# Kernel optimization log

Hardware: AMD Instinct MI355X
Metric: run time of the kernel (lower is better)

## Reference

```python
import jax, jax.numpy as jnp
import numpy as np

N_NODES = 100000
N_EDGES = 600000
D_FEAT = 128
OUT_DIM = 128


def setup_inputs() -> dict:
    key = jax.random.key(0)
    k_x, k_r, k_c, k_v, k_w = jax.random.split(key, 5)
    x = jax.random.normal(k_x, (N_NODES, D_FEAT), dtype=jnp.float32)
    adj_rows = jax.random.randint(k_r, (N_EDGES,), 0, N_NODES, dtype=jnp.int64 if jax.config.jax_enable_x64 else jnp.int32).astype(jnp.int32)
    adj_cols = jax.random.randint(k_c, (N_EDGES,), 0, N_NODES, dtype=jnp.int32)
    adj_vals = jax.random.uniform(k_v, (N_EDGES,), dtype=jnp.float32)
    # Xavier-uniform init for W of shape [2*d, out]
    fan_in, fan_out = 2 * D_FEAT, OUT_DIM
    bound = float(np.sqrt(6.0 / (fan_in + fan_out)))
    W = jax.random.uniform(k_w, (2 * D_FEAT, OUT_DIM), minval=-bound, maxval=bound, dtype=jnp.float32)
    return {"x": x, "adj_rows": adj_rows, "adj_cols": adj_cols, "adj_vals": adj_vals, "W": W}


def reference(x, adj_rows, adj_cols, adj_vals, W):
    # h = A @ x  via COO SpMM: gather neighbor features, scale, segment-sum by row
    msgs = adj_vals[:, None] * x[adj_cols]            # [E, d]
    h = jax.ops.segment_sum(msgs, adj_rows, num_segments=N_NODES)  # [N, d]
    # concat([h, x]) @ W == h @ W[:d] + x @ W[d:]  (avoids materializing concat)
    out = h @ W[:D_FEAT] + x @ W[D_FEAT:]             # [N, out]
    return jax.nn.relu(out)
```

## Files before the change

kernel.cpp:

```cpp
#include <hip/hip_runtime.h>
#include <hip/hip_bf16.h>

constexpr int N_NODES = 100000;
constexpr int N_EDGES = 600000;
constexpr int D = 128;
constexpr int CAP = 32;

constexpr size_t X16_OFF  = 0;
constexpr size_t WP_OFF   = 25600000;
constexpr size_t CNT_OFF  = 25665536;
constexpr size_t BINS_OFF = 26065536;

typedef __attribute__((ext_vector_type(8))) short short8;
typedef __attribute__((ext_vector_type(4))) float float4v;
typedef __attribute__((ext_vector_type(4))) float float4e;
typedef __attribute__((ext_vector_type(4))) int   int4e;

__device__ inline unsigned short f2bf(float f) {
    union { float f; unsigned int u; } v; v.f = f;
    unsigned int u = v.u + 0x7fffu + ((v.u >> 16) & 1u);
    return (unsigned short)(u >> 16);
}
__device__ inline float bf2f(unsigned int lo16) {
    union { unsigned int u; float f; } v; v.u = lo16 << 16;
    return v.f;
}

__global__ __launch_bounds__(256) void prep_cast_kernel(
    const float* __restrict__ x, uint4* __restrict__ x16,
    const float* __restrict__ W, unsigned short* __restrict__ Wp)
{
    const int tid = blockIdx.x * 256 + threadIdx.x;
    const int T   = gridDim.x * 256;

    for (int idx = tid; idx < 8 * 8 * 64 * 8; idx += T) {
        int j    = idx & 7;
        int lane = (idx >> 3) & 63;
        int jt   = (idx >> 9) & 7;
        int s    = idx >> 12;
        int k = s * 32 + (lane >> 4) * 8 + j;
        int n = jt * 16 + (lane & 15);
        Wp[idx] = f2bf(W[k * 128 + n]);
    }

    for (int g = tid; g < N_NODES * D / 8; g += T) {
        const float4e* xp = reinterpret_cast<const float4e*>(x + (size_t)g * 8);
        float4e a = __builtin_nontemporal_load(xp);
        float4e c = __builtin_nontemporal_load(xp + 1);
        uint4 o;
        o.x = (unsigned int)f2bf(a.x) | ((unsigned int)f2bf(a.y) << 16);
        o.y = (unsigned int)f2bf(a.z) | ((unsigned int)f2bf(a.w) << 16);
        o.z = (unsigned int)f2bf(c.x) | ((unsigned int)f2bf(c.y) << 16);
        o.w = (unsigned int)f2bf(c.z) | ((unsigned int)f2bf(c.w) << 16);
        x16[g] = o;
    }
}

__global__ __launch_bounds__(256) void prep_bin_kernel(
    const int* __restrict__ rows, const int* __restrict__ cols,
    const float* __restrict__ vals,
    int* __restrict__ cnt, int2* __restrict__ bins)
{
    const int tid = blockIdx.x * 256 + threadIdx.x;
    const int T   = gridDim.x * 256;

    for (int e = tid; e < N_EDGES; e += T) {
        int r = __builtin_nontemporal_load(rows + e);
        int c = __builtin_nontemporal_load(cols + e);
        float v = __builtin_nontemporal_load(vals + e);
        int pos = atomicAdd(&cnt[r], 1);
        if (pos < CAP)
            bins[(size_t)r * CAP + pos] = make_int2(c, __float_as_int(v));
    }
}

__global__ __launch_bounds__(256) void fused_agg_gemm_kernel(
    const uint4* __restrict__ x16v,
    const unsigned short* __restrict__ x16s,
    const int* __restrict__ cnt,
    const int2* __restrict__ bins,
    const unsigned short* __restrict__ Wp,
    float* __restrict__ out)
{
    __shared__ uint4 lds4[256];

    const int tid  = threadIdx.x;
    const int wave = tid >> 6;
    const int lane = tid & 63;
    const int row0 = blockIdx.x * 16;

    {
        const int G  = wave * 4 + (lane >> 4);
        const int gl = lane & 15;
        const int n  = row0 + G;

        const int4e* b2 = reinterpret_cast<const int4e*>(bins + (size_t)n * CAP);
        const int  d   = cnt[n];
        const int4e c0 = __builtin_nontemporal_load(b2 + 0);
        const int4e c1 = __builtin_nontemporal_load(b2 + 1);
        const int4e c2 = __builtin_nontemporal_load(b2 + 2);
        const int4e c3 = __builtin_nontemporal_load(b2 + 3);
        const int dend = d > CAP ? CAP : d;

        int col0 = c0.x; col0 = col0 < 0 ? 0 : col0;
        col0 = col0 >= N_NODES ? N_NODES - 1 : col0;
        const int cc1 = (1 < dend) ? c0.z : col0;
        const int cc2 = (2 < dend) ? c1.x : col0;
        const int cc3 = (3 < dend) ? c1.z : col0;
        const int cc4 = (4 < dend) ? c2.x : col0;
        const int cc5 = (5 < dend) ? c2.z : col0;
        const int cc6 = (6 < dend) ? c3.x : col0;
        const int cc7 = (7 < dend) ? c3.z : col0;
        const float v0 = (0 < dend) ? __int_as_float(c0.y) : 0.f;
        const float v1 = (1 < dend) ? __int_as_float(c0.w) : 0.f;
        const float v2 = (2 < dend) ? __int_as_float(c1.y) : 0.f;
        const float v3 = (3 < dend) ? __int_as_float(c1.w) : 0.f;
        const float v4 = (4 < dend) ? __int_as_float(c2.y) : 0.f;
        const float v5 = (5 < dend) ? __int_as_float(c2.w) : 0.f;
        const float v6 = (6 < dend) ? __int_as_float(c3.y) : 0.f;
        const float v7 = (7 < dend) ? __int_as_float(c3.w) : 0.f;

        const uint4 p0 = x16v[(size_t)col0 * 16 + gl];
        const uint4 p1 = x16v[(size_t)cc1  * 16 + gl];
        const uint4 p2 = x16v[(size_t)cc2  * 16 + gl];
        const uint4 p3 = x16v[(size_t)cc3  * 16 + gl];
        const uint4 p4 = x16v[(size_t)cc4  * 16 + gl];
        const uint4 p5 = x16v[(size_t)cc5  * 16 + gl];
        const uint4 p6 = x16v[(size_t)cc6  * 16 + gl];
        const uint4 p7 = x16v[(size_t)cc7  * 16 + gl];

        float a0, a1, a2, a3, a4, a5, a6, a7;
        a0  = v0 * bf2f(p0.x & 0xffffu) + v1 * bf2f(p1.x & 0xffffu)
            + v2 * bf2f(p2.x & 0xffffu) + v3 * bf2f(p3.x & 0xffffu)
            + v4 * bf2f(p4.x & 0xffffu) + v5 * bf2f(p5.x & 0xffffu)
            + v6 * bf2f(p6.x & 0xffffu) + v7 * bf2f(p7.x & 0xffffu);
        a1  = v0 * bf2f(p0.x >> 16)     + v1 * bf2f(p1.x >> 16)
            + v2 * bf2f(p2.x >> 16)     + v3 * bf2f(p3.x >> 16)
            + v4 * bf2f(p4.x >> 16)     + v5 * bf2f(p5.x >> 16)
            + v6 * bf2f(p6.x >> 16)     + v7 * bf2f(p7.x >> 16);
        a2  = v0 * bf2f(p0.y & 0xffffu) + v1 * bf2f(p1.y & 0xffffu)
            + v2 * bf2f(p2.y & 0xffffu) + v3 * bf2f(p3.y & 0xffffu)
            + v4 * bf2f(p4.y & 0xffffu) + v5 * bf2f(p5.y & 0xffffu)
            + v6 * bf2f(p6.y & 0xffffu) + v7 * bf2f(p7.y & 0xffffu);
        a3  = v0 * bf2f(p0.y >> 16)     + v1 * bf2f(p1.y >> 16)
            + v2 * bf2f(p2.y >> 16)     + v3 * bf2f(p3.y >> 16)
            + v4 * bf2f(p4.y >> 16)     + v5 * bf2f(p5.y >> 16)
            + v6 * bf2f(p6.y >> 16)     + v7 * bf2f(p7.y >> 16);
        a4  = v0 * bf2f(p0.z & 0xffffu) + v1 * bf2f(p1.z & 0xffffu)
            + v2 * bf2f(p2.z & 0xffffu) + v3 * bf2f(p3.z & 0xffffu)
            + v4 * bf2f(p4.z & 0xffffu) + v5 * bf2f(p5.z & 0xffffu)
            + v6 * bf2f(p6.z & 0xffffu) + v7 * bf2f(p7.z & 0xffffu);
        a5  = v0 * bf2f(p0.z >> 16)     + v1 * bf2f(p1.z >> 16)
            + v2 * bf2f(p2.z >> 16)     + v3 * bf2f(p3.z >> 16)
            + v4 * bf2f(p4.z >> 16)     + v5 * bf2f(p5.z >> 16)
            + v6 * bf2f(p6.z >> 16)     + v7 * bf2f(p7.z >> 16);
        a6  = v0 * bf2f(p0.w & 0xffffu) + v1 * bf2f(p1.w & 0xffffu)
            + v2 * bf2f(p2.w & 0xffffu) + v3 * bf2f(p3.w & 0xffffu)
            + v4 * bf2f(p4.w & 0xffffu) + v5 * bf2f(p5.w & 0xffffu)
            + v6 * bf2f(p6.w & 0xffffu) + v7 * bf2f(p7.w & 0xffffu);
        a7  = v0 * bf2f(p0.w >> 16)     + v1 * bf2f(p1.w >> 16)
            + v2 * bf2f(p2.w >> 16)     + v3 * bf2f(p3.w >> 16)
            + v4 * bf2f(p4.w >> 16)     + v5 * bf2f(p5.w >> 16)
            + v6 * bf2f(p6.w >> 16)     + v7 * bf2f(p7.w >> 16);

        if (dend > 8) {
            const int2* bp = bins + (size_t)n * CAP;
            for (int i = 8; i < dend; i += 4) {
                const int i1 = (i + 1 < dend) ? i + 1 : dend - 1;
                const int i2 = (i + 2 < dend) ? i + 2 : dend - 1;
                const int i3 = (i + 3 < dend) ? i + 3 : dend - 1;
                int2 e0 = bp[i];
                int2 e1 = bp[i1];
                int2 e2 = bp[i2];
                int2 e3 = bp[i3];
                uint4 q0 = x16v[(size_t)e0.x * 16 + gl];
                uint4 q1 = x16v[(size_t)e1.x * 16 + gl];
                uint4 q2 = x16v[(size_t)e2.x * 16 + gl];
                uint4 q3 = x16v[(size_t)e3.x * 16 + gl];
                float w0 = __int_as_float(e0.y);
                float w1 = (i + 1 < dend) ? __int_as_float(e1.y) : 0.f;
                float w2 = (i + 2 < dend) ? __int_as_float(e2.y) : 0.f;
                float w3 = (i + 3 < dend) ? __int_as_float(e3.y) : 0.f;
                a0 += w0 * bf2f(q0.x & 0xffffu) + w1 * bf2f(q1.x & 0xffffu)
                    + w2 * bf2f(q2.x & 0xffffu) + w3 * bf2f(q3.x & 0xffffu);
                a1 += w0 * bf2f(q0.x >> 16)     + w1 * bf2f(q1.x >> 16)
                    + w2 * bf2f(q2.x >> 16)     + w3 * bf2f(q3.x >> 16);
                a2 += w0 * bf2f(q0.y & 0xffffu) + w1 * bf2f(q1.y & 0xffffu)
                    + w2 * bf2f(q2.y & 0xffffu) + w3 * bf2f(q3.y & 0xffffu);
                a3 += w0 * bf2f(q0.y >> 16)     + w1 * bf2f(q1.y >> 16)
                    + w2 * bf2f(q2.y >> 16)     + w3 * bf2f(q3.y >> 16);
                a4 += w0 * bf2f(q0.z & 0xffffu) + w1 * bf2f(q1.z & 0xffffu)
                    + w2 * bf2f(q2.z & 0xffffu) + w3 * bf2f(q3.z & 0xffffu);
                a5 += w0 * bf2f(q0.z >> 16)     + w1 * bf2f(q1.z >> 16)
                    + w2 * bf2f(q2.z >> 16)     + w3 * bf2f(q3.z >> 16);
                a6 += w0 * bf2f(q0.w & 0xffffu) + w1 * bf2f(q1.w & 0xffffu)
                    + w2 * bf2f(q2.w & 0xffffu) + w3 * bf2f(q3.w & 0xffffu);
                a7 += w0 * bf2f(q0.w >> 16)     + w1 * bf2f(q1.w >> 16)
                    + w2 * bf2f(q2.w >> 16)     + w3 * bf2f(q3.w >> 16);
            }
        }

        uint4 o;
        o.x = (unsigned int)f2bf(a0) | ((unsigned int)f2bf(a1) << 16);
        o.y = (unsigned int)f2bf(a2) | ((unsigned int)f2bf(a3) << 16);
        o.z = (unsigned int)f2bf(a4) | ((unsigned int)f2bf(a5) << 16);
        o.w = (unsigned int)f2bf(a6) | ((unsigned int)f2bf(a7) << 16);
        lds4[(gl >> 2) * 64 + G * 4 + (gl & 3)] = o;
    }
    __syncthreads();

    const int m    = lane & 15;
    const int quad = lane >> 4;
    const int jt0  = wave * 2;
    const int jt1  = jt0 + 1;

    const unsigned short* xrow = x16s + (size_t)(row0 + m) * D + quad * 8;

    float4v acc0 = (float4v){0.f, 0.f, 0.f, 0.f};
    float4v acc1 = (float4v){0.f, 0.f, 0.f, 0.f};

    #pragma unroll
    for (int s = 0; s < 8; s++) {
        short8 a;
        if (s < 4)
            a = *reinterpret_cast<const short8*>(&lds4[s * 64 + m * 4 + quad]);
        else
            a = *reinterpret_cast<const short8*>(xrow + (s - 4) * 32);
        short8 b0 = *reinterpret_cast<const short8*>(
            Wp + ((size_t)((s * 8 + jt0) * 64 + lane)) * 8);
        short8 b1 = *reinterpret_cast<const short8*>(
            Wp + ((size_t)((s * 8 + jt1) * 64 + lane)) * 8);
        acc0 = __builtin_amdgcn_mfma_f32_16x16x32_bf16(a, b0, acc0, 0, 0, 0);
        acc1 = __builtin_amdgcn_mfma_f32_16x16x32_bf16(a, b1, acc1, 0, 0, 0);
    }

    #pragma unroll
    for (int reg = 0; reg < 4; reg++) {
        const int r = row0 + quad * 4 + reg;
        float* orow = out + (size_t)r * D;
        __builtin_nontemporal_store(fmaxf(acc0[reg], 0.f), orow + jt0 * 16 + m);
        __builtin_nontemporal_store(fmaxf(acc1[reg], 0.f), orow + jt1 * 16 + m);
    }
}

extern "C" void kernel_launch(void* const* d_in, const int* in_sizes, int n_in,
                              void* d_out, int out_size, void* d_ws, size_t ws_size,
                              hipStream_t stream)
{
    const float* x    = (const float*)d_in[0];
    const int*   rows = (const int*)  d_in[1];
    const int*   cols = (const int*)  d_in[2];
    const float* vals = (const float*)d_in[3];
    const float* W    = (const float*)d_in[4];
    float* out = (float*)d_out;

    char* ws = (char*)d_ws;
    uint4*          x16v = (uint4*)         (ws + X16_OFF);
    unsigned short* x16s = (unsigned short*)(ws + X16_OFF);
    unsigned short* Wp   = (unsigned short*)(ws + WP_OFF);
    int*            cnt  = (int*)           (ws + CNT_OFF);
    int2*           bins = (int2*)          (ws + BINS_OFF);

    hipMemsetAsync(cnt, 0, N_NODES * sizeof(int), stream);
    prep_cast_kernel<<<2048, 256, 0, stream>>>(x, x16v, W, Wp);
    prep_bin_kernel<<<2048, 256, 0, stream>>>(rows, cols, vals, cnt, bins);
    fused_agg_gemm_kernel<<<N_NODES / 16, 256, 0, stream>>>(
        x16v, x16s, cnt, bins, Wp, out);
}
```

Measured before the change: 197.3 us.

## Merge binning and aggregation into a persistent kernel with a grid barrier

The separate memset, binning and fused aggregate+GEMM launches become two kernels. The count zeroing moves into the prep kernel, and binning plus aggregation/GEMM run in one persistent kernel of 1024 blocks, joined by a software grid-wide barrier built on atomics. This is meant to remove launch overhead and kernel boundaries. In exchange, correctness depends on all 1024 blocks being co-resident (launch bounds of 4 blocks per CU are requested), the spin-wait barrier adds cost, and the tile loop now uses fewer blocks than the previous 6250-block launch.

```diff
diff --git a/kernel.cpp b/kernel.cpp
--- a/kernel.cpp
+++ b/kernel.cpp
@@ -5,11 +5,13 @@
 constexpr int N_EDGES = 600000;
 constexpr int D = 128;
 constexpr int CAP = 32;
+constexpr int NB2 = 1024;
 
 constexpr size_t X16_OFF  = 0;
 constexpr size_t WP_OFF   = 25600000;
 constexpr size_t CNT_OFF  = 25665536;
 constexpr size_t BINS_OFF = 26065536;
+constexpr size_t BAR_OFF  = 51665536;
 
 typedef __attribute__((ext_vector_type(8))) short short8;
 typedef __attribute__((ext_vector_type(4))) float float4v;
@@ -26,12 +28,16 @@
     return v.f;
 }
 
-__global__ __launch_bounds__(256) void prep_cast_kernel(
+__global__ __launch_bounds__(256) void prep_kernel(
     const float* __restrict__ x, uint4* __restrict__ x16,
-    const float* __restrict__ W, unsigned short* __restrict__ Wp)
+    const float* __restrict__ W, unsigned short* __restrict__ Wp,
+    int* __restrict__ cnt, int* __restrict__ bar)
 {
     const int tid = blockIdx.x * 256 + threadIdx.x;
     const int T   = gridDim.x * 256;
+
+    if (tid < 2) bar[tid] = 0;
+    for (int i = tid; i < N_NODES; i += T) cnt[i] = 0;
 
     for (int idx = tid; idx < 8 * 8 * 64 * 8; idx += T) {
         int j    = idx & 7;
@@ -56,13 +62,18 @@
     }
 }
 
-__global__ __launch_bounds__(256) void prep_bin_kernel(
+__global__ __launch_bounds__(256, 4) void work_kernel(
     const int* __restrict__ rows, const int* __restrict__ cols,
     const float* __restrict__ vals,
-    int* __restrict__ cnt, int2* __restrict__ bins)
+    const uint4* __restrict__ x16v, const unsigned short* __restrict__ x16s,
+    const unsigned short* __restrict__ Wp,
+    int* __restrict__ cnt, int2* __restrict__ bins,
+    int* __restrict__ bar, float* __restrict__ out)
 {
+    __shared__ uint4 lds4[256];
+
     const int tid = blockIdx.x * 256 + threadIdx.x;
-    const int T   = gridDim.x * 256;
+    const int T   = NB2 * 256;
 
     for (int e = tid; e < N_EDGES; e += T) {
         int r = __builtin_nontemporal_load(rows + e);
@@ -72,174 +83,184 @@
         if (pos < CAP)
             bins[(size_t)r * CAP + pos] = make_int2(c, __float_as_int(v));
     }
-}
-
-__global__ __launch_bounds__(256) void fused_agg_gemm_kernel(
-    const uint4* __restrict__ x16v,
-    const unsigned short* __restrict__ x16s,
-    const int* __restrict__ cnt,
-    const int2* __restrict__ bins,
-    const unsigned short* __restrict__ Wp,
-    float* __restrict__ out)
-{
-    __shared__ uint4 lds4[256];
-
-    const int tid  = threadIdx.x;
-    const int wave = tid >> 6;
-    const int lane = tid & 63;
-    const int row0 = blockIdx.x * 16;
-
-    {
-        const int G  = wave * 4 + (lane >> 4);
-        const int gl = lane & 15;
-        const int n  = row0 + G;
-
-        const int4e* b2 = reinterpret_cast<const int4e*>(bins + (size_t)n * CAP);
-        const int  d   = cnt[n];
-        const int4e c0 = __builtin_nontemporal_load(b2 + 0);
-        const int4e c1 = __builtin_nontemporal_load(b2 + 1);
-        const int4e c2 = __builtin_nontemporal_load(b2 + 2);
-        const int4e c3 = __builtin_nontemporal_load(b2 + 3);
-        const int dend = d > CAP ? CAP : d;
-
-        int col0 = c0.x; col0 = col0 < 0 ? 0 : col0;
-        col0 = col0 >= N_NODES ? N_NODES - 1 : col0;
-        const int cc1 = (1 < dend) ? c0.z : col0;
-        const int cc2 = (2 < dend) ? c1.x : col0;
-        const int cc3 = (3 < dend) ? c1.z : col0;
-        const int cc4 = (4 < dend) ? c2.x : col0;
-        const int cc5 = (5 < dend) ? c2.z : col0;
-        const int cc6 = (6 < dend) ? c3.x : col0;
-        const int cc7 = (7 < dend) ? c3.z : col0;
-        const float v0 = (0 < dend) ? __int_as_float(c0.y) : 0.f;
-        const float v1 = (1 < dend) ? __int_as_float(c0.w) : 0.f;
-        const float v2 = (2 < dend) ? __int_as_float(c1.y) : 0.f;
-        const float v3 = (3 < dend) ? __int_as_float(c1.w) : 0.f;
-        const float v4 = (4 < dend) ? __int_as_float(c2.y) : 0.f;
-        const float v5 = (5 < dend) ? __int_as_float(c2.w) : 0.f;
-        const float v6 = (6 < dend) ? __int_as_float(c3.y) : 0.f;
-        const float v7 = (7 < dend) ? __int_as_float(c3.w) : 0.f;
-
-        const uint4 p0 = x16v[(size_t)col0 * 16 + gl];
-        const uint4 p1 = x16v[(size_t)cc1  * 16 + gl];
-        const uint4 p2 = x16v[(size_t)cc2  * 16 + gl];
-        const uint4 p3 = x16v[(size_t)cc3  * 16 + gl];
-        const uint4 p4 = x16v[(size_t)cc4  * 16 + gl];
-        const uint4 p5 = x16v[(size_t)cc5  * 16 + gl];
-        const uint4 p6 = x16v[(size_t)cc6  * 16 + gl];
-        const uint4 p7 = x16v[(size_t)cc7  * 16 + gl];
-
-        float a0, a1, a2, a3, a4, a5, a6, a7;
-        a0  = v0 * bf2f(p0.x & 0xffffu) + v1 * bf2f(p1.x & 0xffffu)
-            + v2 * bf2f(p2.x & 0xffffu) + v3 * bf2f(p3.x & 0xffffu)
-            + v4 * bf2f(p4.x & 0xffffu) + v5 * bf2f(p5.x & 0xffffu)
-            + v6 * bf2f(p6.x & 0xffffu) + v7 * bf2f(p7.x & 0xffffu);
-        a1  = v0 * bf2f(p0.x >> 16)     + v1 * bf2f(p1.x >> 16)
-            + v2 * bf2f(p2.x >> 16)     + v3 * bf2f(p3.x >> 16)
-            + v4 * bf2f(p4.x >> 16)     + v5 * bf2f(p5.x >> 16)
-            + v6 * bf2f(p6.x >> 16)     + v7 * bf2f(p7.x >> 16);
-        a2  = v0 * bf2f(p0.y & 0xffffu) + v1 * bf2f(p1.y & 0xffffu)
-            + v2 * bf2f(p2.y & 0xffffu) + v3 * bf2f(p3.y & 0xffffu)
-            + v4 * bf2f(p4.y & 0xffffu) + v5 * bf2f(p5.y & 0xffffu)
-            + v6 * bf2f(p6.y & 0xffffu) + v7 * bf2f(p7.y & 0xffffu);
-        a3  = v0 * bf2f(p0.y >> 16)     + v1 * bf2f(p1.y >> 16)
-            + v2 * bf2f(p2.y >> 16)     + v3 * bf2f(p3.y >> 16)
-            + v4 * bf2f(p4.y >> 16)     + v5 * bf2f(p5.y >> 16)
-            + v6 * bf2f(p6.y >> 16)     + v7 * bf2f(p7.y >> 16);
-        a4  = v0 * bf2f(p0.z & 0xffffu) + v1 * bf2f(p1.z & 0xffffu)
-            + v2 * bf2f(p2.z & 0xffffu) + v3 * bf2f(p3.z & 0xffffu)
-            + v4 * bf2f(p4.z & 0xffffu) + v5 * bf2f(p5.z & 0xffffu)
-            + v6 * bf2f(p6.z & 0xffffu) + v7 * bf2f(p7.z & 0xffffu);
-        a5  = v0 * bf2f(p0.z >> 16)     + v1 * bf2f(p1.z >> 16)
-            + v2 * bf2f(p2.z >> 16)     + v3 * bf2f(p3.z >> 16)
-            + v4 * bf2f(p4.z >> 16)     + v5 * bf2f(p5.z >> 16)
-            + v6 * bf2f(p6.z >> 16)     + v7 * bf2f(p7.z >> 16);
-        a6  = v0 * bf2f(p0.w & 0xffffu) + v1 * bf2f(p1.w & 0xffffu)
-            + v2 * bf2f(p2.w & 0xffffu) + v3 * bf2f(p3.w & 0xffffu)
-            + v4 * bf2f(p4.w & 0xffffu) + v5 * bf2f(p5.w & 0xffffu)
-            + v6 * bf2f(p6.w & 0xffffu) + v7 * bf2f(p7.w & 0xffffu);
-        a7  = v0 * bf2f(p0.w >> 16)     + v1 * bf2f(p1.w >> 16)
-            + v2 * bf2f(p2.w >> 16)     + v3 * bf2f(p3.w >> 16)
-            + v4 * bf2f(p4.w >> 16)     + v5 * bf2f(p5.w >> 16)
-            + v6 * bf2f(p6.w >> 16)     + v7 * bf2f(p7.w >> 16);
-
-        if (dend > 8) {
-            const int2* bp = bins + (size_t)n * CAP;
-            for (int i = 8; i < dend; i += 4) {
-                const int i1 = (i + 1 < dend) ? i + 1 : dend - 1;
-                const int i2 = (i + 2 < dend) ? i + 2 : dend - 1;
-                const int i3 = (i + 3 < dend) ? i + 3 : dend - 1;
-                int2 e0 = bp[i];
-                int2 e1 = bp[i1];
-                int2 e2 = bp[i2];
-                int2 e3 = bp[i3];
-                uint4 q0 = x16v[(size_t)e0.x * 16 + gl];
-                uint4 q1 = x16v[(size_t)e1.x * 16 + gl];
-                uint4 q2 = x16v[(size_t)e2.x * 16 + gl];
-                uint4 q3 = x16v[(size_t)e3.x * 16 + gl];
-                float w0 = __int_as_float(e0.y);
-                float w1 = (i + 1 < dend) ? __int_as_float(e1.y) : 0.f;
-                float w2 = (i + 2 < dend) ? __int_as_float(e2.y) : 0.f;
-                float w3 = (i + 3 < dend) ? __int_as_float(e3.y) : 0.f;
-                a0 += w0 * bf2f(q0.x & 0xffffu) + w1 * bf2f(q1.x & 0xffffu)
-                    + w2 * bf2f(q2.x & 0xffffu) + w3 * bf2f(q3.x & 0xffffu);
-                a1 += w0 * bf2f(q0.x >> 16)     + w1 * bf2f(q1.x >> 16)
-                    + w2 * bf2f(q2.x >> 16)     + w3 * bf2f(q3.x >> 16);
-                a2 += w0 * bf2f(q0.y & 0xffffu) + w1 * bf2f(q1.y & 0xffffu)
-                    + w2 * bf2f(q2.y & 0xffffu) + w3 * bf2f(q3.y & 0xffffu);
-                a3 += w0 * bf2f(q0.y >> 16)     + w1 * bf2f(q1.y >> 16)
-                    + w2 * bf2f(q2.y >> 16)     + w3 * bf2f(q3.y >> 16);
-                a4 += w0 * bf2f(q0.z & 0xffffu) + w1 * bf2f(q1.z & 0xffffu)
-                    + w2 * bf2f(q2.z & 0xffffu) + w3 * bf2f(q3.z & 0xffffu);
-                a5 += w0 * bf2f(q0.z >> 16)     + w1 * bf2f(q1.z >> 16)
-                    + w2 * bf2f(q2.z >> 16)     + w3 * bf2f(q3.z >> 16);
-                a6 += w0 * bf2f(q0.w & 0xffffu) + w1 * bf2f(q1.w & 0xffffu)
-                    + w2 * bf2f(q2.w & 0xffffu) + w3 * bf2f(q3.w & 0xffffu);
-                a7 += w0 * bf2f(q0.w >> 16)     + w1 * bf2f(q1.w >> 16)
-                    + w2 * bf2f(q2.w >> 16)     + w3 * bf2f(q3.w >> 16);
+
+    __syncthreads();
+    if (threadIdx.x == 0) {
+        __threadfence();
+        int t = atomicAdd(&bar[0], 1);
+        if (t == NB2 - 1) {
+            __hip_atomic_store(&bar[1], 1, __ATOMIC_RELEASE,
+                               __HIP_MEMORY_SCOPE_AGENT);
+        } else {
+            while (__hip_atomic_load(&bar[1], __ATOMIC_RELAXED,
+                                     __HIP_MEMORY_SCOPE_AGENT) == 0)
+                __builtin_amdgcn_s_sleep(10);
+        }
+    }
+    __syncthreads();
+    __threadfence();
+
+    const int wave = threadIdx.x >> 6;
+    const int lane = threadIdx.x & 63;
+
+    for (int tile = blockIdx.x; tile < N_NODES / 16; tile += NB2) {
+        const int row0 = tile * 16;
+
+        {
+            const int G  = wave * 4 + (lane >> 4);
+            const int gl = lane & 15;
+            const int n  = row0 + G;
+
+            const int4e* b2 = reinterpret_cast<const int4e*>(bins + (size_t)n * CAP);
+            const int  d   = cnt[n];
+            const int4e c0 = __builtin_nontemporal_load(b2 + 0);
+            const int4e c1 = __builtin_nontemporal_load(b2 + 1);
+            const int4e c2 = __builtin_nontemporal_load(b2 + 2);
+            const int4e c3 = __builtin_nontemporal_load(b2 + 3);
+            const int dend = d > CAP ? CAP : d;
+
+            int col0 = c0.x; col0 = col0 < 0 ? 0 : col0;
+            col0 = col0 >= N_NODES ? N_NODES - 1 : col0;
+            const int cc1 = (1 < dend) ? c0.z : col0;
+            const int cc2 = (2 < dend) ? c1.x : col0;
+            const int cc3 = (3 < dend) ? c1.z : col0;
+            const int cc4 = (4 < dend) ? c2.x : col0;
+            const int cc5 = (5 < dend) ? c2.z : col0;
+            const int cc6 = (6 < dend) ? c3.x : col0;
+            const int cc7 = (7 < dend) ? c3.z : col0;
+            const float v0 = (0 < dend) ? __int_as_float(c0.y) : 0.f;
+            const float v1 = (1 < dend) ? __int_as_float(c0.w) : 0.f;
+            const float v2 = (2 < dend) ? __int_as_float(c1.y) : 0.f;
+            const float v3 = (3 < dend) ? __int_as_float(c1.w) : 0.f;
+            const float v4 = (4 < dend) ? __int_as_float(c2.y) : 0.f;
+            const float v5 = (5 < dend) ? __int_as_float(c2.w) : 0.f;
+            const float v6 = (6 < dend) ? __int_as_float(c3.y) : 0.f;
+            const float v7 = (7 < dend) ? __int_as_float(c3.w) : 0.f;
+
+            const uint4 p0 = x16v[(size_t)col0 * 16 + gl];
+            const uint4 p1 = x16v[(size_t)cc1  * 16 + gl];
+            const uint4 p2 = x16v[(size_t)cc2  * 16 + gl];
+            const uint4 p3 = x16v[(size_t)cc3  * 16 + gl];
+            const uint4 p4 = x16v[(size_t)cc4  * 16 + gl];
+            const uint4 p5 = x16v[(size_t)cc5  * 16 + gl];
+            const uint4 p6 = x16v[(size_t)cc6  * 16 + gl];
+            const uint4 p7 = x16v[(size_t)cc7  * 16 + gl];
+
+            float a0, a1, a2, a3, a4, a5, a6, a7;
+            a0  = v0 * bf2f(p0.x & 0xffffu) + v1 * bf2f(p1.x & 0xffffu)
+                + v2 * bf2f(p2.x & 0xffffu) + v3 * bf2f(p3.x & 0xffffu)
+                + v4 * bf2f(p4.x & 0xffffu) + v5 * bf2f(p5.x & 0xffffu)
+                + v6 * bf2f(p6.x & 0xffffu) + v7 * bf2f(p7.x & 0xffffu);
+            a1  = v0 * bf2f(p0.x >> 16)     + v1 * bf2f(p1.x >> 16)
+                + v2 * bf2f(p2.x >> 16)     + v3 * bf2f(p3.x >> 16)
+                + v4 * bf2f(p4.x >> 16)     + v5 * bf2f(p5.x >> 16)
+                + v6 * bf2f(p6.x >> 16)     + v7 * bf2f(p7.x >> 16);
+            a2  = v0 * bf2f(p0.y & 0xffffu) + v1 * bf2f(p1.y & 0xffffu)
+                + v2 * bf2f(p2.y & 0xffffu) + v3 * bf2f(p3.y & 0xffffu)
+                + v4 * bf2f(p4.y & 0xffffu) + v5 * bf2f(p5.y & 0xffffu)
+                + v6 * bf2f(p6.y & 0xffffu) + v7 * bf2f(p7.y & 0xffffu);
+            a3  = v0 * bf2f(p0.y >> 16)     + v1 * bf2f(p1.y >> 16)
+                + v2 * bf2f(p2.y >> 16)     + v3 * bf2f(p3.y >> 16)
+                + v4 * bf2f(p4.y >> 16)     + v5 * bf2f(p5.y >> 16)
+                + v6 * bf2f(p6.y >> 16)     + v7 * bf2f(p7.y >> 16);
+            a4  = v0 * bf2f(p0.z & 0xffffu) + v1 * bf2f(p1.z & 0xffffu)
+                + v2 * bf2f(p2.z & 0xffffu) + v3 * bf2f(p3.z & 0xffffu)
+                + v4 * bf2f(p4.z & 0xffffu) + v5 * bf2f(p5.z & 0xffffu)
+                + v6 * bf2f(p6.z & 0xffffu) + v7 * bf2f(p7.z & 0xffffu);
+            a5  = v0 * bf2f(p0.z >> 16)     + v1 * bf2f(p1.z >> 16)
+                + v2 * bf2f(p2.z >> 16)     + v3 * bf2f(p3.z >> 16)
+                + v4 * bf2f(p4.z >> 16)     + v5 * bf2f(p5.z >> 16)
+                + v6 * bf2f(p6.z >> 16)     + v7 * bf2f(p7.z >> 16);
+            a6  = v0 * bf2f(p0.w & 0xffffu) + v1 * bf2f(p1.w & 0xffffu)
+                + v2 * bf2f(p2.w & 0xffffu) + v3 * bf2f(p3.w & 0xffffu)
+                + v4 * bf2f(p4.w & 0xffffu) + v5 * bf2f(p5.w & 0xffffu)
+                + v6 * bf2f(p6.w & 0xffffu) + v7 * bf2f(p7.w & 0xffffu);
+            a7  = v0 * bf2f(p0.w >> 16)     + v1 * bf2f(p1.w >> 16)
+                + v2 * bf2f(p2.w >> 16)     + v3 * bf2f(p3.w >> 16)
+                + v4 * bf2f(p4.w >> 16)     + v5 * bf2f(p5.w >> 16)
+                + v6 * bf2f(p6.w >> 16)     + v7 * bf2f(p7.w >> 16);
+
+            if (dend > 8) {
+                const int2* bp = bins + (size_t)n * CAP;
+                for (int i = 8; i < dend; i += 4) {
+                    const int i1 = (i + 1 < dend) ? i + 1 : dend - 1;
+                    const int i2 = (i + 2 < dend) ? i + 2 : dend - 1;
+                    const int i3 = (i + 3 < dend) ? i + 3 : dend - 1;
+                    int2 e0 = bp[i];
+                    int2 e1 = bp[i1];
+                    int2 e2 = bp[i2];
+                    int2 e3 = bp[i3];
+                    uint4 q0 = x16v[(size_t)e0.x * 16 + gl];
+                    uint4 q1 = x16v[(size_t)e1.x * 16 + gl];
+                    uint4 q2 = x16v[(size_t)e2.x * 16 + gl];
+                    uint4 q3 = x16v[(size_t)e3.x * 16 + gl];
+                    float w0 = __int_as_float(e0.y);
+                    float w1 = (i + 1 < dend) ? __int_as_float(e1.y) : 0.f;
+                    float w2 = (i + 2 < dend) ? __int_as_float(e2.y) : 0.f;
+                    float w3 = (i + 3 < dend) ? __int_as_float(e3.y) : 0.f;
+                    a0 += w0 * bf2f(q0.x & 0xffffu) + w1 * bf2f(q1.x & 0xffffu)
+                        + w2 * bf2f(q2.x & 0xffffu) + w3 * bf2f(q3.x & 0xffffu);
+                    a1 += w0 * bf2f(q0.x >> 16)     + w1 * bf2f(q1.x >> 16)
+                        + w2 * bf2f(q2.x >> 16)     + w3 * bf2f(q3.x >> 16);
+                    a2 += w0 * bf2f(q0.y & 0xffffu) + w1 * bf2f(q1.y & 0xffffu)
+                        + w2 * bf2f(q2.y & 0xffffu) + w3 * bf2f(q3.y & 0xffffu);
+                    a3 += w0 * bf2f(q0.y >> 16)     + w1 * bf2f(q1.y >> 16)
+                        + w2 * bf2f(q2.y >> 16)     + w3 * bf2f(q3.y >> 16);
+                    a4 += w0 * bf2f(q0.z & 0xffffu) + w1 * bf2f(q1.z & 0xffffu)
+                        + w2 * bf2f(q2.z & 0xffffu) + w3 * bf2f(q3.z & 0xffffu);
+                    a5 += w0 * bf2f(q0.z >> 16)     + w1 * bf2f(q1.z >> 16)
+                        + w2 * bf2f(q2.z >> 16)     + w3 * bf2f(q3.z >> 16);
+                    a6 += w0 * bf2f(q0.w & 0xffffu) + w1 * bf2f(q1.w & 0xffffu)
+                        + w2 * bf2f(q2.w & 0xffffu) + w3 * bf2f(q3.w & 0xffffu);
+                    a7 += w0 * bf2f(q0.w >> 16)     + w1 * bf2f(q1.w >> 16)
+                        + w2 * bf2f(q2.w >> 16)     + w3 * bf2f(q3.w >> 16);
+                }
+            }
+
+            uint4 o;
+            o.x = (unsigned int)f2bf(a0) | ((unsigned int)f2bf(a1) << 16);
+            o.y = (unsigned int)f2bf(a2) | ((unsigned int)f2bf(a3) << 16);
+            o.z = (unsigned int)f2bf(a4) | ((unsigned int)f2bf(a5) << 16);
+            o.w = (unsigned int)f2bf(a6) | ((unsigned int)f2bf(a7) << 16);
+            lds4[(gl >> 2) * 64 + G * 4 + (gl & 3)] = o;
+        }
+        __syncthreads();
+
+        {
+            const int m    = lane & 15;
+            const int quad = lane >> 4;
+            const int jt0  = wave * 2;
+            const int jt1  = jt0 + 1;
+
+            const unsigned short* xrow = x16s + (size_t)(row0 + m) * D + quad * 8;
+
+            float4v acc0 = (float4v){0.f, 0.f, 0.f, 0.f};
+            float4v acc1 = (float4v){0.f, 0.f, 0.f, 0.f};
+
+            #pragma unroll
+            for (int s = 0; s < 8; s++) {
+                short8 a;
+                if (s < 4)
+                    a = *reinterpret_cast<const short8*>(&lds4[s * 64 + m * 4 + quad]);
+                else
+                    a = *reinterpret_cast<const short8*>(xrow + (s - 4) * 32);
+                short8 b0 = *reinterpret_cast<const short8*>(
+                    Wp + ((size_t)((s * 8 + jt0) * 64 + lane)) * 8);
+                short8 b1 = *reinterpret_cast<const short8*>(
+                    Wp + ((size_t)((s * 8 + jt1) * 64 + lane)) * 8);
+                acc0 = __builtin_amdgcn_mfma_f32_16x16x32_bf16(a, b0, acc0, 0, 0, 0);
+                acc1 = __builtin_amdgcn_mfma_f32_16x16x32_bf16(a, b1, acc1, 0, 0, 0);
+            }
+
+            #pragma unroll
+            for (int reg = 0; reg < 4; reg++) {
+                const int r = row0 + quad * 4 + reg;
+                float* orow = out + (size_t)r * D;
+                __builtin_nontemporal_store(fmaxf(acc0[reg], 0.f), orow + jt0 * 16 + m);
+                __builtin_nontemporal_store(fmaxf(acc1[reg], 0.f), orow + jt1 * 16 + m);
             }
         }
-
-        uint4 o;
-        o.x = (unsigned int)f2bf(a0) | ((unsigned int)f2bf(a1) << 16);
-        o.y = (unsigned int)f2bf(a2) | ((unsigned int)f2bf(a3) << 16);
-        o.z = (unsigned int)f2bf(a4) | ((unsigned int)f2bf(a5) << 16);
-        o.w = (unsigned int)f2bf(a6) | ((unsigned int)f2bf(a7) << 16);
-        lds4[(gl >> 2) * 64 + G * 4 + (gl & 3)] = o;
-    }
-    __syncthreads();
-
-    const int m    = lane & 15;
-    const int quad = lane >> 4;
-    const int jt0  = wave * 2;
-    const int jt1  = jt0 + 1;
-
-    const unsigned short* xrow = x16s + (size_t)(row0 + m) * D + quad * 8;
-
-    float4v acc0 = (float4v){0.f, 0.f, 0.f, 0.f};
-    float4v acc1 = (float4v){0.f, 0.f, 0.f, 0.f};
-
-    #pragma unroll
-    for (int s = 0; s < 8; s++) {
-        short8 a;
-        if (s < 4)
-            a = *reinterpret_cast<const short8*>(&lds4[s * 64 + m * 4 + quad]);
-        else
-            a = *reinterpret_cast<const short8*>(xrow + (s - 4) * 32);
-        short8 b0 = *reinterpret_cast<const short8*>(
-            Wp + ((size_t)((s * 8 + jt0) * 64 + lane)) * 8);
-        short8 b1 = *reinterpret_cast<const short8*>(
-            Wp + ((size_t)((s * 8 + jt1) * 64 + lane)) * 8);
-        acc0 = __builtin_amdgcn_mfma_f32_16x16x32_bf16(a, b0, acc0, 0, 0, 0);
-        acc1 = __builtin_amdgcn_mfma_f32_16x16x32_bf16(a, b1, acc1, 0, 0, 0);
-    }
-
-    #pragma unroll
-    for (int reg = 0; reg < 4; reg++) {
-        const int r = row0 + quad * 4 + reg;
-        float* orow = out + (size_t)r * D;
-        __builtin_nontemporal_store(fmaxf(acc0[reg], 0.f), orow + jt0 * 16 + m);
-        __builtin_nontemporal_store(fmaxf(acc1[reg], 0.f), orow + jt1 * 16 + m);
+        __syncthreads();
     }
 }
 
@@ -256,14 +277,13 @@
 
     char* ws = (char*)d_ws;
     uint4*          x16v = (uint4*)         (ws + X16_OFF);
-    unsigned short* x16s = (unsigned short*)(ws + X16_OFF);
+    const unsigned short* x16s = (const unsigned short*)(ws + X16_OFF);
     unsigned short* Wp   = (unsigned short*)(ws + WP_OFF);
     int*            cnt  = (int*)           (ws + CNT_OFF);
     int2*           bins = (int2*)          (ws + BINS_OFF);
-
-    hipMemsetAsync(cnt, 0, N_NODES * sizeof(int), stream);
-    prep_cast_kernel<<<2048, 256, 0, stream>>>(x, x16v, W, Wp);
-    prep_bin_kernel<<<2048, 256, 0, stream>>>(rows, cols, vals, cnt, bins);
-    fused_agg_gemm_kernel<<<N_NODES / 16, 256, 0, stream>>>(
-        x16v, x16s, cnt, bins, Wp, out);
-}
+    int*            bar  = (int*)           (ws + BAR_OFF);
+
+    prep_kernel<<<2048, 256, 0, stream>>>(x, x16v, W, Wp, cnt, bar);
+    work_kernel<<<NB2, 256, 0, stream>>>(rows, cols, vals, x16v, x16s, Wp,
+                                         cnt, bins, bar, out);
+}
```

Result: slower. 367.7 us (+86.4%).
